# Kernel optimization log

Hardware: AMD Instinct MI355X
Metric: run time of the kernel (lower is better)

Reference implementation:

```python
import jax, jax.numpy as jnp
import numpy as np

N = 100_000      # nodes
E = 1_600_000    # edges
D = 128          # hidden_channels
L = 3            # num_layers
G = 5_000        # number of subgraphs (batch ids)
MAXZ = 1_000     # max_z


def setup_inputs() -> dict:
    key = jax.random.key(0)
    ks = jax.random.split(key, 8)
    s = 1.0 / np.sqrt(D)
    return {
        "z": jax.random.randint(ks[0], (N,), 0, MAXZ, dtype=jnp.int32),
        "edge_index": jax.random.randint(ks[1], (2, E), 0, N, dtype=jnp.int32),
        # sorted graph ids, G segments of equal size (each subgraph has >=2 nodes)
        "batch": (jnp.arange(N) * G // N).astype(jnp.int32),
        "z_table": jax.random.normal(ks[2], (MAXZ, D), dtype=jnp.float32) * s,
        "Wl": jax.random.normal(ks[3], (L, D, D), dtype=jnp.float32) * s,
        "bl": jnp.zeros((L, D), jnp.float32),
        "Wr": jax.random.normal(ks[4], (L, D, D), dtype=jnp.float32) * s,
        "W1": jax.random.normal(ks[5], (D, D), dtype=jnp.float32) * s,
        "b1": jnp.zeros((D,), jnp.float32),
        "W2": jax.random.normal(ks[6], (1, D), dtype=jnp.float32) * s,
        "b2": jnp.zeros((1,), jnp.float32),
    }


def reference(z, edge_index, batch, z_table, Wl, bl, Wr, W1, b1, W2, b2):
    src, dst = edge_index[0], edge_index[1]
    x = z_table[z]  # [N, D] z-label embedding (use_feature=False, no node_embedding)

    # in-degree for mean aggregation (shared across layers)
    counts = jax.ops.segment_sum(jnp.ones((E,), x.dtype), dst, num_segments=N)
    inv_deg = 1.0 / jnp.maximum(counts, 1.0)  # [N]

    for l in range(L):
        # SAGEConv: mean-aggregate neighbor features, then lin_l(agg) + lin_r(x)
        agg = jax.ops.segment_sum(x[src], dst, num_segments=N) * inv_deg[:, None]
        x = agg @ Wl[l].T + bl[l] + x @ Wr[l].T
        if l < L - 1:
            x = jax.nn.relu(x)  # dropout is identity in eval mode

    # first node index of each sorted batch segment (np.unique return_index equiv.)
    centers = jnp.searchsorted(batch, jnp.arange(G))  # [G]
    h = x[centers] * x[centers + 1]                   # pairwise center product
    h = jax.nn.relu(h @ W1.T + b1)
    return h @ W2.T + b2  # [G, 1]
```

## Files before the change

kernel.cpp:

```cpp
#include <hip/hip_runtime.h>
#include <hip/hip_bf16.h>
#include <hip/hip_fp16.h>

#define D 128
#define NL 3
#define NODE_SH 8
#define NB_MAX 512
#define BIN_CHUNK 4096

typedef __attribute__((ext_vector_type(8))) short short8;
typedef __attribute__((ext_vector_type(4))) float f32x4;

static inline size_t align256(size_t x){ return (x + 255) & ~(size_t)255; }

static __device__ inline unsigned short f2bf_hi(float f){
    __hip_bfloat16 h = __float2bfloat16(f);
    return *reinterpret_cast<unsigned short*>(&h);
}
static __device__ inline float bf2f(unsigned short u){
    return __uint_as_float(((unsigned)u) << 16);
}

__global__ __launch_bounds__(256) void k_embed(const int* __restrict__ z, const float* __restrict__ zt,
                                               float* __restrict__ x, __half* __restrict__ xh, int N){
    int i = blockIdx.x * blockDim.x + threadIdx.x;
    int n = i >> 5, q = i & 31;
    if (n >= N) return;
    float4 v = *(const float4*)&zt[(size_t)z[n] * D + q * 4];
    *(float4*)&x[(size_t)n * D + q * 4] = v;
    __half2 p0 = __floats2half2_rn(v.x, v.y);
    __half2 p1 = __floats2half2_rn(v.z, v.w);
    uint2 u;
    u.x = *reinterpret_cast<unsigned*>(&p0);
    u.y = *reinterpret_cast<unsigned*>(&p1);
    *(uint2*)&xh[(size_t)n * D + q * 4] = u;
}

__global__ __launch_bounds__(256) void k_bcount(const int* __restrict__ dst, int* __restrict__ bcnt,
                                                int E, int NB){
    __shared__ int h[NB_MAX];
    const int t = threadIdx.x;
    for (int b = t; b < NB_MAX; b += 256) h[b] = 0;
    __syncthreads();
    const int stride = gridDim.x * 256;
    for (int e = blockIdx.x * 256 + t; e < E; e += stride)
        atomicAdd(&h[dst[e] >> NODE_SH], 1);
    __syncthreads();
    for (int b = t; b < NB; b += 256){
        int v = h[b];
        if (v) atomicAdd(&bcnt[b], v);
    }
}

__global__ __launch_bounds__(512) void k_bscan(const int* __restrict__ bcnt, int* __restrict__ gbase,
                                               int* __restrict__ gcur, int* __restrict__ offs,
                                               int NB, int N, int E){
    __shared__ int s[512];
    int t = threadIdx.x;
    int v = (t < NB) ? bcnt[t] : 0;
    s[t] = v; __syncthreads();
    for (int st = 1; st < 512; st <<= 1){
        int u = (t >= st) ? s[t - st] : 0;
        __syncthreads();
        s[t] += u;
        __syncthreads();
    }
    if (t < NB){
        int base = s[t] - v;
        gbase[t] = base;
        gcur[t] = base;
    }
    if (t == 0){ gbase[NB] = E; offs[N] = E; }
}

__global__ __launch_bounds__(256) void k_binA(const int* __restrict__ src, const int* __restrict__ dst,
                                              int* __restrict__ gcur, int* __restrict__ ebuf2,
                                              int E, int NB){
    __shared__ int s_hist[NB_MAX];
    __shared__ int s_lofs[NB_MAX];
    __shared__ int s_delta[NB_MAX];
    __shared__ int s_pack[BIN_CHUNK];
    __shared__ int s_gdst[BIN_CHUNK];
    __shared__ int s_scan[256];
    const int t = threadIdx.x;
    const int e0 = blockIdx.x * BIN_CHUNK;
    for (int b = t; b < NB_MAX; b += 256) s_hist[b] = 0;
    __syncthreads();
    int my_pack[16], my_b[16], my_rank[16];
    #pragma unroll
    for (int i = 0; i < 16; ++i){
        int e = e0 + i * 256 + t;
        if (e < E){
            int s = src[e], d = dst[e];
            int b = d >> NODE_SH;
            my_pack[i] = s | ((d & 255) << 17);
            my_b[i] = b;
            my_rank[i] = atomicAdd(&s_hist[b], 1);
        } else my_b[i] = -1;
    }
    __syncthreads();
    int h0 = s_hist[2 * t], h1 = s_hist[2 * t + 1];
    int sum2 = h0 + h1;
    s_scan[t] = sum2;
    __syncthreads();
    for (int st = 1; st < 256; st <<= 1){
        int v = (t >= st) ? s_scan[t - st] : 0;
        __syncthreads();
        s_scan[t] += v;
        __syncthreads();
    }
    int excl = s_scan[t] - sum2;
    s_lofs[2 * t] = excl;
    s_lofs[2 * t + 1] = excl + h0;
    __syncthreads();
    for (int b = t; b < NB; b += 256){
        int h = s_hist[b];
        int base = (h > 0) ? atomicAdd(&gcur[b], h) : 0;
        s_delta[b] = base - s_lofs[b];
    }
    __syncthreads();
    #pragma unroll
    for (int i = 0; i < 16; ++i){
        if (my_b[i] >= 0){
            int j = s_lofs[my_b[i]] + my_rank[i];
            s_pack[j] = my_pack[i];
            s_gdst[j] = j + s_delta[my_b[i]];
        }
    }
    __syncthreads();
    const int cnt = min(BIN_CHUNK, E - e0);
    for (int j = t; j < cnt; j += 256)
        ebuf2[s_gdst[j]] = s_pack[j];
}

__global__ __launch_bounds__(256) void k_binB(const int* __restrict__ ebuf2, const int* __restrict__ gbase,
                                              int* __restrict__ ebuf, int* __restrict__ offs,
                                              float* __restrict__ invdeg, int N){
    __shared__ int cnt[256];
    __shared__ int lcur[256];
    __shared__ int s_scan[256];
    const int b = blockIdx.x, t = threadIdx.x;
    const int n0 = b << NODE_SH;
    const int rs = gbase[b], re = gbase[b + 1];
    cnt[t] = 0;
    __syncthreads();
    for (int i = rs + t; i < re; i += 256)
        atomicAdd(&cnt[ebuf2[i] >> 17], 1);
    __syncthreads();
    const int c = cnt[t];
    s_scan[t] = c;
    __syncthreads();
    for (int st = 1; st < 256; st <<= 1){
        int u = (t >= st) ? s_scan[t - st] : 0;
        __syncthreads();
        s_scan[t] += u;
        __syncthreads();
    }
    const int excl = s_scan[t] - c;
    lcur[t] = rs + excl;
    if (n0 + t < N){
        offs[n0 + t]   = rs + excl;
        invdeg[n0 + t] = 1.0f / (float)max(c, 1);
    }
    __syncthreads();
    for (int i = rs + t; i < re; i += 256){
        int v = ebuf2[i];
        int p = atomicAdd(&lcur[v >> 17], 1);
        ebuf[p] = v & 0x1FFFF;
    }
}

__global__ __launch_bounds__(256) void k_centers(const int* __restrict__ batch, int* __restrict__ centers, int N){
    int n = blockIdx.x * blockDim.x + threadIdx.x;
    if (n < N && (n == 0 || batch[n] != batch[n - 1])) centers[batch[n]] = n;
}

__global__ __launch_bounds__(256) void k_prepW(const float* __restrict__ Wl, const float* __restrict__ Wr,
                                               const float* __restrict__ W1, float* __restrict__ W1T,
                                               unsigned short* __restrict__ WFh, unsigned short* __restrict__ WFl){
    int i = blockIdx.x * blockDim.x + threadIdx.x;
    if (i < NL * 8 * 8 * 64){
        int lane = i & 63;
        int r = i >> 6;
        int fn = r & 7; r >>= 3;
        int ks = r & 7; r >>= 3;
        int l = r;
        int col = fn * 16 + (lane & 15);
        int k0 = ks * 32 + (lane >> 4) * 8;
        short8 hh, ll;
        #pragma unroll
        for (int j = 0; j < 8; ++j){
            int k = k0 + j;
            float w = (k < D) ? Wl[(size_t)l * D * D + col * D + k]
                              : Wr[(size_t)l * D * D + col * D + (k - D)];
            unsigned short h = f2bf_hi(w);
            hh[j] = (short)h;
            ll[j] = (short)f2bf_hi(w - bf2f(h));
        }
        *(short8*)&WFh[(size_t)i * 8] = hh;
        *(short8*)&WFl[(size_t)i * 8] = ll;
    }
    if (i < D * D){ int k = i / D, d = i % D; W1T[i] = W1[d * D + k]; }
}

static __device__ inline void acc_h4(float4& a, uint2 u){
    __half2 h0 = *reinterpret_cast<__half2*>(&u.x);
    __half2 h1 = *reinterpret_cast<__half2*>(&u.y);
    float2 f0 = __half22float2(h0);
    float2 f1 = __half22float2(h1);
    a.x += f0.x; a.y += f0.y; a.z += f1.x; a.w += f1.y;
}

__global__ __launch_bounds__(256) void k_agg(const __half* __restrict__ xh, const int* __restrict__ ebuf,
                                             const int* __restrict__ offs, const float* __restrict__ invdeg,
                                             float* __restrict__ agg, int N){
    int node = blockIdx.x * 8 + (threadIdx.x >> 5);
    if (node >= N) return;
    int lane = threadIdx.x & 31;
    int s = offs[node], e = offs[node + 1];
    float4 a0 = make_float4(0.f,0.f,0.f,0.f), a1 = a0, a2 = a0, a3 = a0;
    int i = s;
    for (; i + 4 <= e; i += 4){
        int nb0 = ebuf[i], nb1 = ebuf[i+1], nb2 = ebuf[i+2], nb3 = ebuf[i+3];
        uint2 u0 = *(const uint2*)&xh[(size_t)nb0 * D + lane * 4];
        uint2 u1 = *(const uint2*)&xh[(size_t)nb1 * D + lane * 4];
        uint2 u2 = *(const uint2*)&xh[(size_t)nb2 * D + lane * 4];
        uint2 u3 = *(const uint2*)&xh[(size_t)nb3 * D + lane * 4];
        acc_h4(a0, u0); acc_h4(a1, u1); acc_h4(a2, u2); acc_h4(a3, u3);
    }
    for (; i < e; ++i){
        uint2 u = *(const uint2*)&xh[(size_t)ebuf[i] * D + lane * 4];
        acc_h4(a0, u);
    }
    a0.x += a1.x + a2.x + a3.x;
    a0.y += a1.y + a2.y + a3.y;
    a0.z += a1.z + a2.z + a3.z;
    a0.w += a1.w + a2.w + a3.w;
    float sc = invdeg[node];
    a0.x *= sc; a0.y *= sc; a0.z *= sc; a0.w *= sc;
    *(float4*)&agg[(size_t)node * D + lane * 4] = a0;
}

template<bool RELU>
__global__ __launch_bounds__(256) void k_dense_mfma(const float* __restrict__ Ag, const float* __restrict__ X,
                                                    const unsigned short* __restrict__ WFh,
                                                    const unsigned short* __restrict__ WFl,
                                                    const float* __restrict__ bias,
                                                    float* __restrict__ Out, __half* __restrict__ XhOut, int N){
    const int wave = threadIdx.x >> 6;
    const int lane = threadIdx.x & 63;
    const int l15  = lane & 15;
    const int kg   = lane >> 4;
    const int rbase = blockIdx.x * 128 + wave * 32;

    f32x4 acc[2][8];
    #pragma unroll
    for (int t = 0; t < 2; ++t)
        #pragma unroll
        for (int fn = 0; fn < 8; ++fn) acc[t][fn] = (f32x4){0.f, 0.f, 0.f, 0.f};

    #pragma unroll
    for (int ks = 0; ks < 8; ++ks){
        const float* S = (ks < 4) ? Ag : X;
        const int ko = (ks & 3) * 32 + kg * 8;
        short8 ah[2], al[2];
        #pragma unroll
        for (int t = 0; t < 2; ++t){
            int row = rbase + t * 16 + l15;
            row = min(row, N - 1);
            const float* ap = &S[(size_t)row * D + ko];
            float4 x0 = *(const float4*)ap;
            float4 x1 = *(const float4*)(ap + 4);
            float av[8] = {x0.x, x0.y, x0.z, x0.w, x1.x, x1.y, x1.z, x1.w};
            #pragma unroll
            for (int j = 0; j < 8; ++j){
                unsigned short h = f2bf_hi(av[j]);
                ah[t][j] = (short)h;
                al[t][j] = (short)f2bf_hi(av[j] - bf2f(h));
            }
        }
        #pragma unroll
        for (int fn = 0; fn < 8; ++fn){
            const size_t fo = ((size_t)(ks * 8 + fn) * 64 + lane) * 8;
            const short8 bh = *(const short8*)&WFh[fo];
            const short8 bl = *(const short8*)&WFl[fo];
            #pragma unroll
            for (int t = 0; t < 2; ++t){
                acc[t][fn] = __builtin_amdgcn_mfma_f32_16x16x32_bf16(ah[t], bh, acc[t][fn], 0, 0, 0);
                acc[t][fn] = __builtin_amdgcn_mfma_f32_16x16x32_bf16(al[t], bh, acc[t][fn], 0, 0, 0);
                acc[t][fn] = __builtin_amdgcn_mfma_f32_16x16x32_bf16(ah[t], bl, acc[t][fn], 0, 0, 0);
            }
        }
    }
    #pragma unroll
    for (int t = 0; t < 2; ++t){
        const int rb = rbase + t * 16 + (kg << 2);
        #pragma unroll
        for (int fn = 0; fn < 8; ++fn){
            const int col = fn * 16 + l15;
            const float bv = bias[col];
            #pragma unroll
            for (int r = 0; r < 4; ++r){
                const int orow = rb + r;
                if (orow < N){
                    float v = acc[t][fn][r] + bv;
                    if (RELU) v = fmaxf(v, 0.f);
                    Out[(size_t)orow * D + col] = v;
                    XhOut[(size_t)orow * D + col] = __float2half(v);
                }
            }
        }
    }
}

__global__ __launch_bounds__(128) void k_head(const float* __restrict__ x, const int* __restrict__ centers,
                                              const float* __restrict__ W1T, const float* __restrict__ b1,
                                              const float* __restrict__ W2, const float* __restrict__ b2,
                                              float* __restrict__ out){
    __shared__ float hs[D];
    __shared__ float red[D];
    int g = blockIdx.x; int d = threadIdx.x;
    int c = centers[g];
    hs[d] = x[(size_t)c * D + d] * x[(size_t)(c + 1) * D + d];
    __syncthreads();
    float acc = b1[d];
    #pragma unroll 8
    for (int k = 0; k < D; ++k) acc = fmaf(hs[k], W1T[k * D + d], acc);
    acc = fmaxf(acc, 0.f);
    red[d] = acc * W2[d];
    __syncthreads();
    for (int st = 64; st > 0; st >>= 1){
        if (d < st) red[d] += red[d + st];
        __syncthreads();
    }
    if (d == 0) out[g] = red[0] + b2[0];
}

extern "C" void kernel_launch(void* const* d_in, const int* in_sizes, int n_in,
                              void* d_out, int out_size, void* d_ws, size_t ws_size,
                              hipStream_t stream){
    const int*   z     = (const int*)  d_in[0];
    const int*   eidx  = (const int*)  d_in[1];
    const int*   batch = (const int*)  d_in[2];
    const float* zt    = (const float*)d_in[3];
    const float* Wl    = (const float*)d_in[4];
    const float* bl    = (const float*)d_in[5];
    const float* Wr    = (const float*)d_in[6];
    const float* W1    = (const float*)d_in[7];
    const float* b1    = (const float*)d_in[8];
    const float* W2    = (const float*)d_in[9];
    const float* b2    = (const float*)d_in[10];
    float* out = (float*)d_out;

    const int N = in_sizes[0];
    const int E = in_sizes[1] / 2;
    const int G = out_size;
    const int NB = (N + 255) >> NODE_SH;
    const int* src  = eidx;
    const int* dstp = eidx + E;

    char* p = (char*)d_ws;
    auto alloc = [&](size_t bytes){ char* r = p; p += align256(bytes); return r; };
    float* xa      = (float*)alloc((size_t)N * D * 4);
    float* xb      = (float*)alloc((size_t)N * D * 4);
    float* agg     = (float*)alloc((size_t)N * D * 4);
    __half* xha    = (__half*)alloc((size_t)N * D * 2);
    __half* xhb    = (__half*)alloc((size_t)N * D * 2);
    float* invdeg  = (float*)alloc((size_t)N * 4);
    int*   offs    = (int*)  alloc((size_t)(N + 1) * 4);
    int*   ebuf    = (int*)  alloc((size_t)E * 4);
    int*   ebuf2   = (int*)  alloc((size_t)E * 4);
    int*   centers = (int*)  alloc((size_t)G * 4);
    int*   bcnt    = (int*)  alloc((size_t)NB_MAX * 4);
    int*   gbase   = (int*)  alloc((size_t)(NB_MAX + 1) * 4);
    int*   gcur    = (int*)  alloc((size_t)NB_MAX * 4);
    float* W1T     = (float*)alloc((size_t)D * D * 4);
    unsigned short* WFh = (unsigned short*)alloc((size_t)NL * 8 * 8 * 64 * 8 * 2);
    unsigned short* WFl = (unsigned short*)alloc((size_t)NL * 8 * 8 * 64 * 8 * 2);
    (void)ws_size; (void)n_in;

    hipMemsetAsync(bcnt, 0, (size_t)NB_MAX * 4, stream);
    k_embed<<<(N * 32 + 255) / 256, 256, 0, stream>>>(z, zt, xa, xha, N);
    k_bcount<<<512, 256, 0, stream>>>(dstp, bcnt, E, NB);
    k_bscan<<<1, 512, 0, stream>>>(bcnt, gbase, gcur, offs, NB, N, E);
    k_binA<<<(E + BIN_CHUNK - 1) / BIN_CHUNK, 256, 0, stream>>>(src, dstp, gcur, ebuf2, E, NB);
    k_binB<<<NB, 256, 0, stream>>>(ebuf2, gbase, ebuf, offs, invdeg, N);
    k_centers<<<(N + 255) / 256, 256, 0, stream>>>(batch, centers, N);
    k_prepW<<<64, 256, 0, stream>>>(Wl, Wr, W1, W1T, WFh, WFl);

    float* xc = xa; float* xn = xb;
    __half* xhc = xha; __half* xhn = xhb;
    for (int l = 0; l < NL; ++l){
        k_agg<<<(N + 7) / 8, 256, 0, stream>>>(xhc, ebuf, offs, invdeg, agg, N);
        const unsigned short* wh = WFh + (size_t)l * 8 * 8 * 64 * 8;
        const unsigned short* wl = WFl + (size_t)l * 8 * 8 * 64 * 8;
        if (l < NL - 1)
            k_dense_mfma<true ><<<(N + 127) / 128, 256, 0, stream>>>(agg, xc, wh, wl, bl + l * D, xn, xhn, N);
        else
            k_dense_mfma<false><<<(N + 127) / 128, 256, 0, stream>>>(agg, xc, wh, wl, bl + l * D, xn, xhn, N);
        float* t = xc; xc = xn; xn = t;
        __half* th = xhc; xhc = xhn; xhn = th;
    }
    k_head<<<G, 128, 0, stream>>>(xc, centers, W1T, b1, W2, b2, out);
}
```

Before: 492.8 us.

## Switch dense layers to fp16 activations with two-term fp16 weight split MFMA

The aggregation output and the dense-layer inputs are now stored as fp16 instead of fp32. The dense kernel feeds them straight into f16 MFMA, using two products (activation times weight-high and weight-low) instead of three bf16 split products. The fp32 copies of intermediate node features are dropped, and only the final layer writes fp32 output. This cuts memory traffic and MFMA count, at the cost of activation precision falling to fp16.

```diff
diff --git a/kernel.cpp b/kernel.cpp
--- a/kernel.cpp
+++ b/kernel.cpp
@@ -9,25 +9,17 @@
 #define BIN_CHUNK 4096
 
 typedef __attribute__((ext_vector_type(8))) short short8;
+typedef __attribute__((ext_vector_type(8))) _Float16 half8;
 typedef __attribute__((ext_vector_type(4))) float f32x4;
 
 static inline size_t align256(size_t x){ return (x + 255) & ~(size_t)255; }
 
-static __device__ inline unsigned short f2bf_hi(float f){
-    __hip_bfloat16 h = __float2bfloat16(f);
-    return *reinterpret_cast<unsigned short*>(&h);
-}
-static __device__ inline float bf2f(unsigned short u){
-    return __uint_as_float(((unsigned)u) << 16);
-}
-
 __global__ __launch_bounds__(256) void k_embed(const int* __restrict__ z, const float* __restrict__ zt,
-                                               float* __restrict__ x, __half* __restrict__ xh, int N){
+                                               __half* __restrict__ xh, int N){
     int i = blockIdx.x * blockDim.x + threadIdx.x;
     int n = i >> 5, q = i & 31;
     if (n >= N) return;
     float4 v = *(const float4*)&zt[(size_t)z[n] * D + q * 4];
-    *(float4*)&x[(size_t)n * D + q * 4] = v;
     __half2 p0 = __floats2half2_rn(v.x, v.y);
     __half2 p1 = __floats2half2_rn(v.z, v.w);
     uint2 u;
@@ -177,7 +169,7 @@
 
 __global__ __launch_bounds__(256) void k_prepW(const float* __restrict__ Wl, const float* __restrict__ Wr,
                                                const float* __restrict__ W1, float* __restrict__ W1T,
-                                               unsigned short* __restrict__ WFh, unsigned short* __restrict__ WFl){
+                                               __half* __restrict__ WFh, __half* __restrict__ WFl){
     int i = blockIdx.x * blockDim.x + threadIdx.x;
     if (i < NL * 8 * 8 * 64){
         int lane = i & 63;
@@ -187,18 +179,21 @@
         int l = r;
         int col = fn * 16 + (lane & 15);
         int k0 = ks * 32 + (lane >> 4) * 8;
-        short8 hh, ll;
+        __half hh[8], ll[8];
         #pragma unroll
         for (int j = 0; j < 8; ++j){
             int k = k0 + j;
             float w = (k < D) ? Wl[(size_t)l * D * D + col * D + k]
                               : Wr[(size_t)l * D * D + col * D + (k - D)];
-            unsigned short h = f2bf_hi(w);
-            hh[j] = (short)h;
-            ll[j] = (short)f2bf_hi(w - bf2f(h));
-        }
-        *(short8*)&WFh[(size_t)i * 8] = hh;
-        *(short8*)&WFl[(size_t)i * 8] = ll;
+            __half h = __float2half(w);
+            hh[j] = h;
+            ll[j] = __float2half(w - __half2float(h));
+        }
+        #pragma unroll
+        for (int j = 0; j < 8; ++j){
+            WFh[(size_t)i * 8 + j] = hh[j];
+            WFl[(size_t)i * 8 + j] = ll[j];
+        }
     }
     if (i < D * D){ int k = i / D, d = i % D; W1T[i] = W1[d * D + k]; }
 }
@@ -213,7 +208,7 @@
 
 __global__ __launch_bounds__(256) void k_agg(const __half* __restrict__ xh, const int* __restrict__ ebuf,
                                              const int* __restrict__ offs, const float* __restrict__ invdeg,
-                                             float* __restrict__ agg, int N){
+                                             __half* __restrict__ aggh, int N){
     int node = blockIdx.x * 8 + (threadIdx.x >> 5);
     if (node >= N) return;
     int lane = threadIdx.x & 31;
@@ -237,14 +232,17 @@
     a0.z += a1.z + a2.z + a3.z;
     a0.w += a1.w + a2.w + a3.w;
     float sc = invdeg[node];
-    a0.x *= sc; a0.y *= sc; a0.z *= sc; a0.w *= sc;
-    *(float4*)&agg[(size_t)node * D + lane * 4] = a0;
-}
-
-template<bool RELU>
-__global__ __launch_bounds__(256) void k_dense_mfma(const float* __restrict__ Ag, const float* __restrict__ X,
-                                                    const unsigned short* __restrict__ WFh,
-                                                    const unsigned short* __restrict__ WFl,
+    __half2 p0 = __floats2half2_rn(a0.x * sc, a0.y * sc);
+    __half2 p1 = __floats2half2_rn(a0.z * sc, a0.w * sc);
+    uint2 u;
+    u.x = *reinterpret_cast<unsigned*>(&p0);
+    u.y = *reinterpret_cast<unsigned*>(&p1);
+    *(uint2*)&aggh[(size_t)node * D + lane * 4] = u;
+}
+
+template<bool FINAL>
+__global__ __launch_bounds__(256) void k_dense_mfma(const __half* __restrict__ Agh, const __half* __restrict__ Xh,
+                                                    const __half* __restrict__ WFh, const __half* __restrict__ WFl,
                                                     const float* __restrict__ bias,
                                                     float* __restrict__ Out, __half* __restrict__ XhOut, int N){
     const int wave = threadIdx.x >> 6;
@@ -261,34 +259,24 @@
 
     #pragma unroll
     for (int ks = 0; ks < 8; ++ks){
-        const float* S = (ks < 4) ? Ag : X;
+        const __half* S = (ks < 4) ? Agh : Xh;
         const int ko = (ks & 3) * 32 + kg * 8;
-        short8 ah[2], al[2];
+        half8 av[2];
         #pragma unroll
         for (int t = 0; t < 2; ++t){
             int row = rbase + t * 16 + l15;
             row = min(row, N - 1);
-            const float* ap = &S[(size_t)row * D + ko];
-            float4 x0 = *(const float4*)ap;
-            float4 x1 = *(const float4*)(ap + 4);
-            float av[8] = {x0.x, x0.y, x0.z, x0.w, x1.x, x1.y, x1.z, x1.w};
-            #pragma unroll
-            for (int j = 0; j < 8; ++j){
-                unsigned short h = f2bf_hi(av[j]);
-                ah[t][j] = (short)h;
-                al[t][j] = (short)f2bf_hi(av[j] - bf2f(h));
-            }
+            av[t] = *(const half8*)&S[(size_t)row * D + ko];
         }
         #pragma unroll
         for (int fn = 0; fn < 8; ++fn){
             const size_t fo = ((size_t)(ks * 8 + fn) * 64 + lane) * 8;
-            const short8 bh = *(const short8*)&WFh[fo];
-            const short8 bl = *(const short8*)&WFl[fo];
+            const half8 bh = *(const half8*)&WFh[fo];
+            const half8 bl = *(const half8*)&WFl[fo];
             #pragma unroll
             for (int t = 0; t < 2; ++t){
-                acc[t][fn] = __builtin_amdgcn_mfma_f32_16x16x32_bf16(ah[t], bh, acc[t][fn], 0, 0, 0);
-                acc[t][fn] = __builtin_amdgcn_mfma_f32_16x16x32_bf16(al[t], bh, acc[t][fn], 0, 0, 0);
-                acc[t][fn] = __builtin_amdgcn_mfma_f32_16x16x32_bf16(ah[t], bl, acc[t][fn], 0, 0, 0);
+                acc[t][fn] = __builtin_amdgcn_mfma_f32_16x16x32_f16(av[t], bh, acc[t][fn], 0, 0, 0);
+                acc[t][fn] = __builtin_amdgcn_mfma_f32_16x16x32_f16(av[t], bl, acc[t][fn], 0, 0, 0);
             }
         }
     }
@@ -304,9 +292,12 @@
                 const int orow = rb + r;
                 if (orow < N){
                     float v = acc[t][fn][r] + bv;
-                    if (RELU) v = fmaxf(v, 0.f);
-                    Out[(size_t)orow * D + col] = v;
-                    XhOut[(size_t)orow * D + col] = __float2half(v);
+                    if (!FINAL){
+                        v = fmaxf(v, 0.f);
+                        XhOut[(size_t)orow * D + col] = __float2half(v);
+                    } else {
+                        Out[(size_t)orow * D + col] = v;
+                    }
                 }
             }
         }
@@ -361,9 +352,8 @@
 
     char* p = (char*)d_ws;
     auto alloc = [&](size_t bytes){ char* r = p; p += align256(bytes); return r; };
-    float* xa      = (float*)alloc((size_t)N * D * 4);
-    float* xb      = (float*)alloc((size_t)N * D * 4);
-    float* agg     = (float*)alloc((size_t)N * D * 4);
+    float*  xf     = (float*)alloc((size_t)N * D * 4);
+    __half* aggh   = (__half*)alloc((size_t)N * D * 2);
     __half* xha    = (__half*)alloc((size_t)N * D * 2);
     __half* xhb    = (__half*)alloc((size_t)N * D * 2);
     float* invdeg  = (float*)alloc((size_t)N * 4);
@@ -375,12 +365,12 @@
     int*   gbase   = (int*)  alloc((size_t)(NB_MAX + 1) * 4);
     int*   gcur    = (int*)  alloc((size_t)NB_MAX * 4);
     float* W1T     = (float*)alloc((size_t)D * D * 4);
-    unsigned short* WFh = (unsigned short*)alloc((size_t)NL * 8 * 8 * 64 * 8 * 2);
-    unsigned short* WFl = (unsigned short*)alloc((size_t)NL * 8 * 8 * 64 * 8 * 2);
+    __half* WFh    = (__half*)alloc((size_t)NL * 8 * 8 * 64 * 8 * 2);
+    __half* WFl    = (__half*)alloc((size_t)NL * 8 * 8 * 64 * 8 * 2);
     (void)ws_size; (void)n_in;
 
     hipMemsetAsync(bcnt, 0, (size_t)NB_MAX * 4, stream);
-    k_embed<<<(N * 32 + 255) / 256, 256, 0, stream>>>(z, zt, xa, xha, N);
+    k_embed<<<(N * 32 + 255) / 256, 256, 0, stream>>>(z, zt, xha, N);
     k_bcount<<<512, 256, 0, stream>>>(dstp, bcnt, E, NB);
     k_bscan<<<1, 512, 0, stream>>>(bcnt, gbase, gcur, offs, NB, N, E);
     k_binA<<<(E + BIN_CHUNK - 1) / BIN_CHUNK, 256, 0, stream>>>(src, dstp, gcur, ebuf2, E, NB);
@@ -388,18 +378,16 @@
     k_centers<<<(N + 255) / 256, 256, 0, stream>>>(batch, centers, N);
     k_prepW<<<64, 256, 0, stream>>>(Wl, Wr, W1, W1T, WFh, WFl);
 
-    float* xc = xa; float* xn = xb;
     __half* xhc = xha; __half* xhn = xhb;
     for (int l = 0; l < NL; ++l){
-        k_agg<<<(N + 7) / 8, 256, 0, stream>>>(xhc, ebuf, offs, invdeg, agg, N);
-        const unsigned short* wh = WFh + (size_t)l * 8 * 8 * 64 * 8;
-        const unsigned short* wl = WFl + (size_t)l * 8 * 8 * 64 * 8;
+        k_agg<<<(N + 7) / 8, 256, 0, stream>>>(xhc, ebuf, offs, invdeg, aggh, N);
+        const __half* wh = WFh + (size_t)l * 8 * 8 * 64 * 8;
+        const __half* wl = WFl + (size_t)l * 8 * 8 * 64 * 8;
         if (l < NL - 1)
-            k_dense_mfma<true ><<<(N + 127) / 128, 256, 0, stream>>>(agg, xc, wh, wl, bl + l * D, xn, xhn, N);
+            k_dense_mfma<false><<<(N + 127) / 128, 256, 0, stream>>>(aggh, xhc, wh, wl, bl + l * D, nullptr, xhn, N);
         else
-            k_dense_mfma<false><<<(N + 127) / 128, 256, 0, stream>>>(agg, xc, wh, wl, bl + l * D, xn, xhn, N);
-        float* t = xc; xc = xn; xn = t;
+            k_dense_mfma<true ><<<(N + 127) / 128, 256, 0, stream>>>(aggh, xhc, wh, wl, bl + l * D, xf, nullptr, N);
         __half* th = xhc; xhc = xhn; xhn = th;
     }
-    k_head<<<G, 128, 0, stream>>>(xc, centers, W1T, b1, W2, b2, out);
-}
+    k_head<<<G, 128, 0, stream>>>(xf, centers, W1T, b1, W2, b2, out);
+}
```

Result: no change. 499.2 us (+1.3%).
